# Performance work log

Hardware: AMD Instinct MI355X
Metric: run time of the kernel (lower is better)

The kernel has to match this reference:

```python
import jax, jax.numpy as jnp
import numpy as np

N = 1_000_000   # num nodes
D = 128         # embedding dimension (order=1, no halving)
T = 100         # number of SGD batches (all with alpha = init_alpha, i.e. b < 100)
B = 1024        # batch_size
K = 6           # 1 positive + negative=5 samples per edge
ALPHA = 0.025   # init_alpha


def setup_inputs() -> dict:
    key = jax.random.key(0)
    k1, k2, k3 = jax.random.split(key, 3)
    # original init: (np.random.random((N, D)) - 0.5) / D
    emb_vertex = (jax.random.uniform(k1, (N, D), dtype=jnp.float32) - 0.5) / D
    u_idx = jax.random.randint(k2, (T, B), 0, N)          # sampled edge sources
    tgt_idx = jax.random.randint(k3, (T, B, K), 0, N)     # col 0: positive v, cols 1..5: negatives
    return {"emb_vertex": emb_vertex, "u_idx": u_idx, "tgt_idx": tgt_idx}


def reference(emb_vertex, u_idx, tgt_idx):
    # labels: positive (j=0) -> 1, negatives -> 0
    label = jnp.zeros((B, K), emb_vertex.dtype).at[:, 0].set(1.0)

    def step(emb, batch):
        u, tgt = batch                                    # [B], [B, K]
        vec_u = emb[u]                                    # [B, D] (numpy fancy-index copy)
        vec_v = emb[tgt]                                  # [B, K, D]
        f = jax.nn.sigmoid(jnp.einsum('bd,bkd->bk', vec_u, vec_v))  # [B, K]
        g = ALPHA * (label - f)                           # [B, K]
        # vec_error accumulated over the 1+negative inner iterations
        vec_error = jnp.einsum('bk,bkd->bd', g, vec_v)    # [B, D]
        # so only emb_vertex[u] += vec_error persists.
        emb = emb.at[u].add(vec_error)
        return emb, None

    emb_final, _ = jax.lax.scan(step, emb_vertex, (u_idx, tgt_idx))
    # final L2 row-normalization (sklearn preprocessing.normalize(emb, 'l2'))
    norm = jnp.maximum(jnp.linalg.norm(emb_final, axis=1, keepdims=True), 1e-12)
    return emb_final / norm
```

## Files before the change

kernel.cpp:

```cpp
#include <hip/hip_runtime.h>

typedef unsigned int uint;

#define N_NODES 1000000
#define D       128
#define T_STEPS 100
#define B       1024
#define K       6
#define ALPHA   0.025f

#define CNBLK  1280
#define CTPB   256
#define CHUNK  10
#define NCHUNK (T_STEPS / CHUNK)
#define CE     (CHUNK * B)
#define NWAVES (CNBLK * CTPB / 64)
#define EPW    (CE / NWAVES)

#define FLAG_OFF     65536
#define CNT_BYTES    ((size_t)FLAG_OFF * 4)
#define SPARSE_BYTES ((size_t)(FLAG_OFF + N_NODES) * 4)

__device__ __forceinline__ float wave_sum(float v) {
#pragma unroll
    for (int off = 32; off; off >>= 1) v += __shfl_xor(v, off, 64);
    return v;
}

__device__ __forceinline__ uint aloadu(const uint* p) {
    return __hip_atomic_load(p, __ATOMIC_RELAXED, __HIP_MEMORY_SCOPE_AGENT);
}

__device__ __forceinline__ void bar_sync_acq(uint* ws_u, int k) {
    __syncthreads();
    if (threadIdx.x == 0)
        atomicAdd(&ws_u[k * 2048 + (int)blockIdx.x], 1u);
    if (threadIdx.x < 64) {
        const uint* s = ws_u + k * 2048 + threadIdx.x;
        for (;;) {
            int got = 0;
#pragma unroll
            for (int i = 0; i < CNBLK / 64; ++i) got += (aloadu(s + i * 64) != 0u);
            if (got == CNBLK / 64) break;
        }
    }
    __syncthreads();
    if (threadIdx.x == 0)
        __builtin_amdgcn_fence(__ATOMIC_ACQUIRE, "agent");
    __syncthreads();
}

template <bool SPARSE>
__global__ __launch_bounds__(256) void prologue(const float* __restrict__ emb_in,
                                                const int*   __restrict__ u_idx,
                                                float*       __restrict__ out,
                                                uint*        __restrict__ flags)
{
    if (SPARSE) {
        const int wave = (blockIdx.x * 256 + threadIdx.x) >> 6;
        const int lane = threadIdx.x & 63;
        const int nw = gridDim.x * 4;
        for (int e = wave; e < T_STEPS * B; e += nw) {
            const int r = u_idx[e];
            if (lane == 0) flags[r] = 1u;
            const size_t off = (size_t)r * D + 2 * lane;
            *(float2*)(out + off) = *(const float2*)(emb_in + off);
        }
    } else {
        const int tid = blockIdx.x * 256 + threadIdx.x;
        const int stride = gridDim.x * 256;
        const float4* src = (const float4*)emb_in;
        float4*       dst = (float4*)out;
        for (int i = tid; i < N_NODES * D / 4; i += stride) dst[i] = src[i];
    }
}

template <bool SPARSE>
__global__ __launch_bounds__(CTPB) void line_loop(const float* __restrict__ emb_in,
                                                  const int*   __restrict__ u_idx,
                                                  const int*   __restrict__ tgt_idx,
                                                  float*       __restrict__ out,
                                                  uint*        ws_u)
{
    const int w    = (blockIdx.x * CTPB + threadIdx.x) >> 6;
    const int lane = threadIdx.x & 63;
    const uint* flags = ws_u + FLAG_OFF;

    for (int c = 0; c < NCHUNK; ++c) {
        int    cu[EPW];
        float2 e2[EPW];
        {
            float2 u2l[EPW];
            float2 v2l[EPW][K];
#pragma unroll
            for (int jj = 0; jj < EPW; ++jj) {
                const int e = c * CE + w + jj * NWAVES;
                const int u = u_idx[e];
                cu[jj] = u;
                u2l[jj] = *(const float2*)(out + (size_t)u * D + 2 * lane);
#pragma unroll
                for (int k = 0; k < K; ++k) {
                    const int v = tgt_idx[e * K + k];
                    const float* src = (SPARSE && !flags[v]) ? emb_in : out;
                    v2l[jj][k] = *(const float2*)(src + (size_t)v * D + 2 * lane);
                }
            }
#pragma unroll
            for (int jj = 0; jj < EPW; ++jj) {
                float2 acc = make_float2(0.f, 0.f);
#pragma unroll
                for (int k = 0; k < K; ++k) {
                    const float s = wave_sum(u2l[jj].x * v2l[jj][k].x +
                                             u2l[jj].y * v2l[jj][k].y);
                    const float f = 1.f / (1.f + __expf(-s));
                    const float gg = ALPHA * ((k == 0 ? 1.f : 0.f) - f);
                    acc.x += gg * v2l[jj][k].x;
                    acc.y += gg * v2l[jj][k].y;
                }
                e2[jj] = acc;
            }
        }

#pragma unroll
        for (int jj = 0; jj < EPW; ++jj) {
            float* urow = out + (size_t)cu[jj] * D + 2 * lane;
            atomicAdd(urow,     e2[jj].x);
            atomicAdd(urow + 1, e2[jj].y);
        }

        if (c + 1 < NCHUNK)
            bar_sync_acq(ws_u, c);
    }
}

template <bool SPARSE>
__global__ __launch_bounds__(256) void normalize_k(const float* __restrict__ emb_in,
                                                   float*       __restrict__ out,
                                                   const uint*  __restrict__ flags)
{
    const int wave = (blockIdx.x * 256 + threadIdx.x) >> 6;
    const int lane = threadIdx.x & 63;
    const int nw = gridDim.x * 4;
    for (int r0 = wave * 4; r0 < N_NODES; r0 += nw * 4) {
        uint4 f4 = SPARSE ? *(const uint4*)(flags + r0) : make_uint4(1u, 1u, 1u, 1u);
        const uint fl[4] = { f4.x, f4.y, f4.z, f4.w };
        float2 v[4];
#pragma unroll
        for (int j = 0; j < 4; ++j) {
            const float* src = fl[j] ? out : emb_in;
            v[j] = *(const float2*)(src + (size_t)(r0 + j) * D + 2 * lane);
        }
#pragma unroll
        for (int j = 0; j < 4; ++j) {
            const float ss  = wave_sum(v[j].x * v[j].x + v[j].y * v[j].y);
            const float inv = 1.f / fmaxf(sqrtf(ss), 1e-12f);
            *(float2*)(out + (size_t)(r0 + j) * D + 2 * lane) =
                make_float2(v[j].x * inv, v[j].y * inv);
        }
    }
}

extern "C" void kernel_launch(void* const* d_in, const int* in_sizes, int n_in,
                              void* d_out, int out_size, void* d_ws, size_t ws_size,
                              hipStream_t stream)
{
    const float* emb_in  = (const float*)d_in[0];
    const int*   u_idx   = (const int*)d_in[1];
    const int*   tgt_idx = (const int*)d_in[2];
    float*       out     = (float*)d_out;
    uint*        ws_u    = (uint*)d_ws;
    uint*        flags   = ws_u + FLAG_OFF;

    const bool sparse = ws_size >= SPARSE_BYTES;
    hipMemsetAsync(d_ws, 0, sparse ? SPARSE_BYTES : CNT_BYTES, stream);

    if (sparse) {
        prologue<true>   <<<1024, 256, 0, stream>>>(emb_in, u_idx, out, flags);
        line_loop<true>  <<<CNBLK, CTPB, 0, stream>>>(emb_in, u_idx, tgt_idx, out, ws_u);
        normalize_k<true><<<2048, 256, 0, stream>>>(emb_in, out, flags);
    } else {
        prologue<false>   <<<2048, 256, 0, stream>>>(emb_in, u_idx, out, flags);
        line_loop<false>  <<<CNBLK, CTPB, 0, stream>>>(emb_in, u_idx, tgt_idx, out, ws_u);
        normalize_k<false><<<2048, 256, 0, stream>>>(emb_in, out, flags);
    }
}
```

Before: 565.1 us.

## Fuse normalization of untouched rows into SGD loop barrier slack

Rows never updated by SGD (unflagged) are now normalized directly from the input inside the persistent SGD kernel. The work is split into slices placed before the compute and between a split barrier arrive and wait, so it overlaps the latency-bound updates and barrier spins. The final normalize pass then only visits flagged rows, avoiding a full-table read-write pass. The cost is extra memory traffic competing with the SGD loop's gathers and atomics.

```diff
diff --git a/kernel.cpp b/kernel.cpp
--- a/kernel.cpp
+++ b/kernel.cpp
@@ -17,6 +17,10 @@
 #define NWAVES (CNBLK * CTPB / 64)
 #define EPW    (CE / NWAVES)
 
+#define RPC     20
+#define SLICE_A 12
+#define SLICE_B 8
+
 #define FLAG_OFF     65536
 #define CNT_BYTES    ((size_t)FLAG_OFF * 4)
 #define SPARSE_BYTES ((size_t)(FLAG_OFF + N_NODES) * 4)
@@ -31,10 +35,41 @@
     return __hip_atomic_load(p, __ATOMIC_RELAXED, __HIP_MEMORY_SCOPE_AGENT);
 }
 
-__device__ __forceinline__ void bar_sync_acq(uint* ws_u, int k) {
+__device__ __forceinline__ void norm_slice(const float* __restrict__ emb_in,
+                                           float* __restrict__ out,
+                                           const uint* __restrict__ flags,
+                                           int lane, int r0, int nrows)
+{
+    for (int j0 = 0; j0 < nrows; j0 += 4) {
+        float2 v[4];
+        int    act[4];
+#pragma unroll
+        for (int j = 0; j < 4; ++j) {
+            const int r = r0 + j0 + j;
+            act[j] = (r < N_NODES) && (flags[r] == 0u);
+            if (act[j])
+                v[j] = *(const float2*)(emb_in + (size_t)r * D + 2 * lane);
+        }
+#pragma unroll
+        for (int j = 0; j < 4; ++j) {
+            if (act[j]) {
+                const float ss  = wave_sum(v[j].x * v[j].x + v[j].y * v[j].y);
+                const float inv = 1.f / fmaxf(sqrtf(ss), 1e-12f);
+                const int r = r0 + j0 + j;
+                *(float2*)(out + (size_t)r * D + 2 * lane) =
+                    make_float2(v[j].x * inv, v[j].y * inv);
+            }
+        }
+    }
+}
+
+__device__ __forceinline__ void bar_arrive(uint* ws_u, int k) {
     __syncthreads();
     if (threadIdx.x == 0)
         atomicAdd(&ws_u[k * 2048 + (int)blockIdx.x], 1u);
+}
+__device__ __forceinline__ void bar_wait_acq(uint* ws_u, int k) {
+    __syncthreads();
     if (threadIdx.x < 64) {
         const uint* s = ws_u + k * 2048 + threadIdx.x;
         for (;;) {
@@ -105,6 +140,11 @@
                     v2l[jj][k] = *(const float2*)(src + (size_t)v * D + 2 * lane);
                 }
             }
+
+            if (SPARSE)
+                norm_slice(emb_in, out, flags, lane,
+                           (c * NWAVES + w) * RPC, SLICE_A);
+
 #pragma unroll
             for (int jj = 0; jj < EPW; ++jj) {
                 float2 acc = make_float2(0.f, 0.f);
@@ -128,34 +168,53 @@
             atomicAdd(urow + 1, e2[jj].y);
         }
 
+        bar_arrive(ws_u, c);
+
+        if (SPARSE)
+            norm_slice(emb_in, out, flags, lane,
+                       (c * NWAVES + w) * RPC + SLICE_A, SLICE_B);
+
         if (c + 1 < NCHUNK)
-            bar_sync_acq(ws_u, c);
-    }
-}
-
-template <bool SPARSE>
-__global__ __launch_bounds__(256) void normalize_k(const float* __restrict__ emb_in,
-                                                   float*       __restrict__ out,
-                                                   const uint*  __restrict__ flags)
+            bar_wait_acq(ws_u, c);
+    }
+}
+
+__global__ __launch_bounds__(256) void normalize_flagged(float* __restrict__ out,
+                                                         const uint* __restrict__ flags)
 {
     const int wave = (blockIdx.x * 256 + threadIdx.x) >> 6;
     const int lane = threadIdx.x & 63;
     const int nw = gridDim.x * 4;
     for (int r0 = wave * 4; r0 < N_NODES; r0 += nw * 4) {
-        uint4 f4 = SPARSE ? *(const uint4*)(flags + r0) : make_uint4(1u, 1u, 1u, 1u);
+        const uint4 f4 = *(const uint4*)(flags + r0);
+        if (!(f4.x | f4.y | f4.z | f4.w)) continue;
         const uint fl[4] = { f4.x, f4.y, f4.z, f4.w };
-        float2 v[4];
-#pragma unroll
-        for (int j = 0; j < 4; ++j) {
-            const float* src = fl[j] ? out : emb_in;
-            v[j] = *(const float2*)(src + (size_t)(r0 + j) * D + 2 * lane);
-        }
-#pragma unroll
-        for (int j = 0; j < 4; ++j) {
-            const float ss  = wave_sum(v[j].x * v[j].x + v[j].y * v[j].y);
+#pragma unroll
+        for (int j = 0; j < 4; ++j) {
+            if (fl[j]) {
+                float2* p = (float2*)(out + (size_t)(r0 + j) * D + 2 * lane);
+                const float2 v = *p;
+                const float ss  = wave_sum(v.x * v.x + v.y * v.y);
+                const float inv = 1.f / fmaxf(sqrtf(ss), 1e-12f);
+                *p = make_float2(v.x * inv, v.y * inv);
+            }
+        }
+    }
+}
+
+__global__ __launch_bounds__(256) void normalize_all(float* __restrict__ out)
+{
+    const int wave = (blockIdx.x * 256 + threadIdx.x) >> 6;
+    const int lane = threadIdx.x & 63;
+    const int nw = gridDim.x * 4;
+    for (int r0 = wave * 4; r0 < N_NODES; r0 += nw * 4) {
+#pragma unroll
+        for (int j = 0; j < 4; ++j) {
+            float2* p = (float2*)(out + (size_t)(r0 + j) * D + 2 * lane);
+            const float2 v = *p;
+            const float ss  = wave_sum(v.x * v.x + v.y * v.y);
             const float inv = 1.f / fmaxf(sqrtf(ss), 1e-12f);
-            *(float2*)(out + (size_t)(r0 + j) * D + 2 * lane) =
-                make_float2(v[j].x * inv, v[j].y * inv);
+            *p = make_float2(v.x * inv, v.y * inv);
         }
     }
 }
@@ -175,12 +234,12 @@
     hipMemsetAsync(d_ws, 0, sparse ? SPARSE_BYTES : CNT_BYTES, stream);
 
     if (sparse) {
-        prologue<true>   <<<1024, 256, 0, stream>>>(emb_in, u_idx, out, flags);
-        line_loop<true>  <<<CNBLK, CTPB, 0, stream>>>(emb_in, u_idx, tgt_idx, out, ws_u);
-        normalize_k<true><<<2048, 256, 0, stream>>>(emb_in, out, flags);
+        prologue<true>  <<<1024, 256, 0, stream>>>(emb_in, u_idx, out, flags);
+        line_loop<true> <<<CNBLK, CTPB, 0, stream>>>(emb_in, u_idx, tgt_idx, out, ws_u);
+        normalize_flagged<<<2048, 256, 0, stream>>>(out, flags);
     } else {
-        prologue<false>   <<<2048, 256, 0, stream>>>(emb_in, u_idx, out, flags);
-        line_loop<false>  <<<CNBLK, CTPB, 0, stream>>>(emb_in, u_idx, tgt_idx, out, ws_u);
-        normalize_k<false><<<2048, 256, 0, stream>>>(emb_in, out, flags);
-    }
-}
+        prologue<false>  <<<2048, 256, 0, stream>>>(emb_in, u_idx, out, flags);
+        line_loop<false> <<<CNBLK, CTPB, 0, stream>>>(emb_in, u_idx, tgt_idx, out, ws_u);
+        normalize_all<<<2048, 256, 0, stream>>>(out);
+    }
+}
```

Result: faster. 544.1 us (-3.7%).
